# Kernel tuning notes

Measured on AMD Instinct MI355X. Metric: run time of the kernel, lower is better.

## Reference

```python
import jax, jax.numpy as jnp
import numpy as np

HID = 2048      # hidden_size
H = 16          # num query heads
KV = 4          # num kv heads
HD = HID // H   # head_dim = 128
THETA = 1000000.0
T = 2048        # tokens (single causal sequence)


def _rope(x, positions):
    # neox-style rotate-half RoPE over full head_dim. x: [T, h, HD]
    half = HD // 2
    inv_freq = THETA ** (-jnp.arange(half, dtype=jnp.float32) * 2.0 / HD)  # [half]
    freqs = positions.astype(jnp.float32)[:, None] * inv_freq              # [T, half]
    cos = jnp.cos(freqs)[:, None, :]
    sin = jnp.sin(freqs)[:, None, :]
    x1, x2 = x[..., :half], x[..., half:]
    return jnp.concatenate([x1 * cos - x2 * sin, x2 * cos + x1 * sin], axis=-1)


def setup_inputs() -> dict:
    key = jax.random.key(0)
    k1, k2, k3 = jax.random.split(key, 3)
    hidden_states = jax.random.normal(k1, (T, HID), jnp.float32) * 0.02
    w_qkv = jax.random.normal(k2, (HID, (H + 2 * KV) * HD), jnp.float32) * 0.02
    w_o = jax.random.normal(k3, (H * HD, HID), jnp.float32) * 0.02
    positions = jnp.arange(T, dtype=jnp.int32)
    return {"hidden_states": hidden_states, "w_qkv": w_qkv, "w_o": w_o,
            "positions": positions}


def reference(hidden_states, w_qkv, w_o, positions):
    q_size, kv_size = H * HD, KV * HD
    qkv = hidden_states @ w_qkv                                  # [T, q+2kv]
    q = qkv[:, :q_size].reshape(T, H, HD)
    k = qkv[:, q_size:q_size + kv_size].reshape(T, KV, HD)
    v = qkv[:, q_size + kv_size:].reshape(T, KV, HD)
    q = _rope(q, positions)
    k = _rope(k, positions)
    # GQA: expand kv heads to query heads
    group = H // KV
    k_e = jnp.repeat(k, group, axis=1)                           # [T, H, HD]
    v_e = jnp.repeat(v, group, axis=1)
    scale = HD ** -0.5
    scores = jnp.einsum('thd,shd->hts', q, k_e) * scale          # [H, T, T]
    causal = positions[:, None] >= positions[None, :]            # [T, T]
    scores = jnp.where(causal[None, :, :], scores, -1e30)
    attn = jax.nn.softmax(scores, axis=-1)
    o = jnp.einsum('hts,shd->thd', attn, v_e).reshape(T, H * HD)
    return o @ w_o
```

## Files before the change

kernel.cpp:

```cpp
#include <hip/hip_runtime.h>
#include <hip/hip_bf16.h>

#define T_LEN 2048
#define HID 2048
#define NH 16
#define NKV 4
#define HD 128
#define QKV_COLS 3072

typedef __attribute__((ext_vector_type(8))) short bf16x8;
typedef __attribute__((ext_vector_type(4))) float f32x4;

static __device__ __forceinline__ ushort f2bf(float f) {
  __hip_bfloat16 h = __float2bfloat16(f);
  return *reinterpret_cast<ushort*>(&h);
}
static __device__ __forceinline__ float bf2f(ushort u) {
  union { unsigned int i; float f; } v;
  v.i = ((unsigned int)u) << 16;
  return v.f;
}

static __device__ __forceinline__ void async_copy16(const ushort* g, ushort* l) {
  __builtin_amdgcn_global_load_lds(
      (const __attribute__((address_space(1))) unsigned int*)g,
      (__attribute__((address_space(3))) unsigned int*)l, 16, 0, 0);
}

__global__ __launch_bounds__(256) void prep(
    const float* __restrict__ hidden, ushort* __restrict__ hb,
    const float* __restrict__ w_qkv, ushort* __restrict__ wqkvT,
    const int* __restrict__ positions, float2* __restrict__ tbl) {
  __shared__ float t[64][65];
  const int b = blockIdx.x;
  const int tid = threadIdx.x;
  if (b < 4096) {
    int idx = (b * 256 + tid) * 4;
    float4 v = *(const float4*)(hidden + idx);
    ushort4 o;
    o.x = f2bf(v.x); o.y = f2bf(v.y); o.z = f2bf(v.z); o.w = f2bf(v.w);
    *(ushort4*)(hb + idx) = o;
  } else if (b < 5632) {
    const int tb = b - 4096;
    const int bk = (tb & 31) * 64, bn = (tb >> 5) * 64;
    const int c = tid & 63;
#pragma unroll
    for (int i = 0; i < 16; ++i) {
      int r = (tid >> 6) + i * 4;
      t[r][c] = w_qkv[(size_t)(bk + r) * QKV_COLS + bn + c];
    }
    __syncthreads();
#pragma unroll
    for (int i = 0; i < 16; ++i) {
      int r = (tid >> 6) + i * 4;
      wqkvT[(size_t)(bn + r) * HID + bk + c] = f2bf(t[c][r]);
    }
  } else {
    const int rb = b - 5632;
    const int tt = rb * 4 + (tid >> 6), j = tid & 63;
    double inv_freq = pow(1000000.0, -(double)(2 * j) / 128.0);
    double ang = (double)positions[tt] * inv_freq;
    double s, c2;
    sincos(ang, &s, &c2);
    tbl[(size_t)tt * 64 + j] = make_float2((float)c2, (float)s);
  }
}

__global__ __launch_bounds__(256) void transpose_cast(
    const float* __restrict__ W, ushort* __restrict__ WT, int K, int N) {
  __shared__ float t[64][65];
  const int bk = blockIdx.x * 64, bn = blockIdx.y * 64;
  const int tid = threadIdx.x;
  const int c = tid & 63;
#pragma unroll
  for (int i = 0; i < 16; ++i) {
    int r = (tid >> 6) + i * 4;
    t[r][c] = W[(size_t)(bk + r) * N + bn + c];
  }
  __syncthreads();
#pragma unroll
  for (int i = 0; i < 16; ++i) {
    int r = (tid >> 6) + i * 4;
    WT[(size_t)(bn + r) * K + bk + c] = f2bf(t[c][r]);
  }
}

template <bool OUT_BF16>
__global__ __launch_bounds__(256, 3) void gemm_bt(
    const ushort* __restrict__ A, const ushort* __restrict__ BT,
    void* __restrict__ C, int M, int N, int K) {
  __shared__ __align__(16) ushort lds[2][1536 * 8];
  const int tid = threadIdx.x;
  const int bm = blockIdx.y * 64, bn = blockIdx.x * 128;
  const int wave = tid >> 6, lane = tid & 63;
  const int lr = lane & 15, lq = lane >> 4;
  const int wm = (wave & 1) * 32, wn = (wave >> 1) * 64;

  f32x4 acc[2][4];
#pragma unroll
  for (int i = 0; i < 2; ++i)
#pragma unroll
    for (int j = 0; j < 4; ++j) {
      acc[i][j][0] = 0.f; acc[i][j][1] = 0.f;
      acc[i][j][2] = 0.f; acc[i][j][3] = 0.f;
    }

  auto stage = [&](int k0, int buf) {
#pragma unroll
    for (int it = 0; it < 2; ++it) {
      int c = it * 256 + tid;
      int row = c >> 3, sl = c & 7, kc = sl ^ (row & 7);
      async_copy16(A + (size_t)(bm + row) * K + k0 + kc * 8, &lds[buf][c * 8]);
    }
#pragma unroll
    for (int it = 0; it < 4; ++it) {
      int c = it * 256 + tid;
      int row = c >> 3, sl = c & 7, kc = sl ^ (row & 7);
      async_copy16(BT + (size_t)(bn + row) * K + k0 + kc * 8,
                   &lds[buf][(512 + c) * 8]);
    }
  };

  stage(0, 0);
  __syncthreads();
  int cur = 0;
  for (int k0 = 0; k0 < K; k0 += 64) {
    if (k0 + 64 < K) stage(k0 + 64, cur ^ 1);
#pragma unroll
    for (int ks = 0; ks < 2; ++ks) {
      bf16x8 af[2], bfr[4];
#pragma unroll
      for (int mi = 0; mi < 2; ++mi) {
        int row = wm + mi * 16 + lr, kc = ks * 4 + lq;
        af[mi] = *(const bf16x8*)&lds[cur][(row * 8 + (kc ^ (row & 7))) * 8];
      }
#pragma unroll
      for (int ni = 0; ni < 4; ++ni) {
        int row = wn + ni * 16 + lr, kc = ks * 4 + lq;
        bfr[ni] =
            *(const bf16x8*)&lds[cur][(512 + row * 8 + (kc ^ (row & 7))) * 8];
      }
#pragma unroll
      for (int mi = 0; mi < 2; ++mi)
#pragma unroll
        for (int ni = 0; ni < 4; ++ni)
          acc[mi][ni] = __builtin_amdgcn_mfma_f32_16x16x32_bf16(
              af[mi], bfr[ni], acc[mi][ni], 0, 0, 0);
    }
    __syncthreads();
    cur ^= 1;
  }

#pragma unroll
  for (int mi = 0; mi < 2; ++mi)
#pragma unroll
    for (int ni = 0; ni < 4; ++ni)
#pragma unroll
      for (int r = 0; r < 4; ++r) {
        size_t row = bm + wm + mi * 16 + lq * 4 + r;
        size_t col = bn + wn + ni * 16 + lr;
        if (OUT_BF16)
          ((ushort*)C)[row * N + col] = f2bf(acc[mi][ni][r]);
        else
          ((float*)C)[row * N + col] = acc[mi][ni][r];
      }
}

__global__ __launch_bounds__(256, 3) void gemm_qkv(
    const ushort* __restrict__ A, const ushort* __restrict__ BT,
    ushort* __restrict__ qkvb, ushort* __restrict__ vt,
    const float2* __restrict__ tbl, int M, int N, int K) {
  __shared__ __align__(16) ushort lds[2][1536 * 8];
  const int tid = threadIdx.x;
  const int bm = blockIdx.y * 64, bn = blockIdx.x * 128;
  const int wave = tid >> 6, lane = tid & 63;
  const int lr = lane & 15, lq = lane >> 4;
  const int wm = (wave & 1) * 32, wn = (wave >> 1) * 64;

  f32x4 acc[2][4];
#pragma unroll
  for (int i = 0; i < 2; ++i)
#pragma unroll
    for (int j = 0; j < 4; ++j) {
      acc[i][j][0] = 0.f; acc[i][j][1] = 0.f;
      acc[i][j][2] = 0.f; acc[i][j][3] = 0.f;
    }

  auto stage = [&](int k0, int buf) {
#pragma unroll
    for (int it = 0; it < 2; ++it) {
      int c = it * 256 + tid;
      int row = c >> 3, sl = c & 7, kc = sl ^ (row & 7);
      async_copy16(A + (size_t)(bm + row) * K + k0 + kc * 8, &lds[buf][c * 8]);
    }
#pragma unroll
    for (int it = 0; it < 4; ++it) {
      int c = it * 256 + tid;
      int row = c >> 3, sl = c & 7, kc = sl ^ (row & 7);
      async_copy16(BT + (size_t)(bn + row) * K + k0 + kc * 8,
                   &lds[buf][(512 + c) * 8]);
    }
  };

  stage(0, 0);
  __syncthreads();
  int cur = 0;
  for (int k0 = 0; k0 < K; k0 += 64) {
    if (k0 + 64 < K) stage(k0 + 64, cur ^ 1);
#pragma unroll
    for (int ks = 0; ks < 2; ++ks) {
      bf16x8 af[2], bfr[4];
#pragma unroll
      for (int mi = 0; mi < 2; ++mi) {
        int row = wm + mi * 16 + lr, kc = ks * 4 + lq;
        af[mi] = *(const bf16x8*)&lds[cur][(row * 8 + (kc ^ (row & 7))) * 8];
      }
#pragma unroll
      for (int ni = 0; ni < 4; ++ni) {
        int row = wn + ni * 16 + lr, kc = ks * 4 + lq;
        bfr[ni] =
            *(const bf16x8*)&lds[cur][(512 + row * 8 + (kc ^ (row & 7))) * 8];
      }
#pragma unroll
      for (int mi = 0; mi < 2; ++mi)
#pragma unroll
        for (int ni = 0; ni < 4; ++ni)
          acc[mi][ni] = __builtin_amdgcn_mfma_f32_16x16x32_bf16(
              af[mi], bfr[ni], acc[mi][ni], 0, 0, 0);
    }
    __syncthreads();
    cur ^= 1;
  }

  const int head = bn >> 7;
  ushort* ep = &lds[0][0];
  if (head < 20) {
#pragma unroll
    for (int mi = 0; mi < 2; ++mi)
#pragma unroll
      for (int ni = 0; ni < 4; ++ni)
#pragma unroll
        for (int r = 0; r < 4; ++r)
          ep[(wm + mi * 16 + lq * 4 + r) * 130 + wn + ni * 16 + lr] =
              f2bf(acc[mi][ni][r]);
    __syncthreads();

    const float qs = (head < NH) ? 0.08838834764831845f : 1.0f;
#pragma unroll
    for (int it = 0; it < 16; ++it) {
      int idx = it * 256 + tid;
      int row = idx >> 6, j = idx & 63;
      float x1 = bf2f(ep[row * 130 + j]);
      float x2 = bf2f(ep[row * 130 + 64 + j]);
      float2 cs = tbl[(size_t)(bm + row) * 64 + j];
      qkvb[(size_t)(bm + row) * QKV_COLS + bn + j] =
          f2bf((x1 * cs.x - x2 * cs.y) * qs);
      qkvb[(size_t)(bm + row) * QKV_COLS + bn + 64 + j] =
          f2bf((x2 * cs.x + x1 * cs.y) * qs);
    }
  } else {
#pragma unroll
    for (int mi = 0; mi < 2; ++mi)
#pragma unroll
      for (int ni = 0; ni < 4; ++ni)
#pragma unroll
        for (int r = 0; r < 4; ++r)
          ep[(wm + mi * 16 + lq * 4 + r) * 130 + wn + ni * 16 + lr] =
              f2bf(acc[mi][ni][r]);
    __syncthreads();

    const int vd0 = bn - 2560;
#pragma unroll
    for (int it = 0; it < 8; ++it) {
      int idx = it * 256 + tid;
      int vd = idx >> 4, tg = (idx & 15) * 4;
      ushort4 w;
      w.x = ep[(tg + 0) * 130 + vd];
      w.y = ep[(tg + 1) * 130 + vd];
      w.z = ep[(tg + 2) * 130 + vd];
      w.w = ep[(tg + 3) * 130 + vd];
      *(ushort4*)&vt[(size_t)(vd0 + vd) * T_LEN + bm + tg] = w;
    }
  }
}

__global__ __launch_bounds__(256, 3) void attn_mfma(
    const ushort* __restrict__ qkv, const ushort* __restrict__ vt,
    ushort* __restrict__ o, ushort* __restrict__ partials,
    float* __restrict__ ml) {
  int qt, h, k_begin, k_end, slot = -1;
  {
    const int i = blockIdx.x;
    if (i < 512) {
      qt = 31 - (i >> 5);
      const int rem = i & 31;
      h = rem >> 1;
      const int chunk = rem & 1;
      const int n = qt + 1, half = n >> 1;
      k_begin = chunk ? half : 0;
      k_end = chunk ? n : half;
      slot = ((qt - 16) * 16 + h) * 2 + chunk;
    } else {
      const int j = i - 512;
      qt = 15 - (j >> 4);
      h = j & 15;
      k_begin = 0;
      k_end = qt + 1;
    }
  }
  const int kh = h >> 2;
  const int tid = threadIdx.x;
  const int wave = tid >> 6, lane = tid & 63;
  const int lr = lane & 15, lq = lane >> 4;
  const int wq = wave >> 1, ws = wave & 1;

  __shared__ __align__(16) ushort KsL[1024 * 8];
  __shared__ __align__(16) ushort VtsL[1024 * 8];
  __shared__ __align__(16) ushort Ps[8 * 67 * 8];
  __shared__ float l_sh[64][2];

  bf16x8 qf[2][4];
  {
    const ushort* qbase =
        qkv + (size_t)(qt * 64 + wq * 32 + lr) * QKV_COLS + h * HD + lq * 8;
#pragma unroll
    for (int mi = 0; mi < 2; ++mi)
#pragma unroll
      for (int kk = 0; kk < 4; ++kk)
        qf[mi][kk] = *(const bf16x8*)(qbase + (size_t)mi * 16 * QKV_COLS + kk * 32);
  }

  float l_part[2][4];
#pragma unroll
  for (int mi = 0; mi < 2; ++mi)
#pragma unroll
    for (int r = 0; r < 4; ++r) l_part[mi][r] = 0.f;
  f32x4 o_acc[4][2];
#pragma unroll
  for (int qi = 0; qi < 4; ++qi)
#pragma unroll
    for (int di = 0; di < 2; ++di) {
      o_acc[qi][di][0] = 0.f; o_acc[qi][di][1] = 0.f;
      o_acc[qi][di][2] = 0.f; o_acc[qi][di][3] = 0.f;
    }

  for (int kt = k_begin; kt < k_end; ++kt) {
    __syncthreads();

    {
      const ushort* kbase = qkv + 2048 + kh * HD;
#pragma unroll
      for (int it = 0; it < 4; ++it) {
        int c = it * 256 + tid;
        int s = c >> 4, sl = c & 15, dg = sl ^ (s & 15);
        async_copy16(kbase + (size_t)(kt * 64 + s) * QKV_COLS + dg * 8,
                     &KsL[c * 8]);
      }
    }
    {
      const ushort* vbase = vt + (size_t)(kh * HD) * T_LEN + kt * 64;
#pragma unroll
      for (int it = 0; it < 4; ++it) {
        int c = it * 256 + tid;
        int d = c >> 3, sl = c & 7, sc = sl ^ (d & 7);
        async_copy16(vbase + (size_t)d * T_LEN + sc * 8, &VtsL[c * 8]);
      }
    }
    __syncthreads();

    f32x4 s_acc[2][2];
#pragma unroll
    for (int mi = 0; mi < 2; ++mi)
#pragma unroll
      for (int ni = 0; ni < 2; ++ni) {
        s_acc[mi][ni][0] = 0.f; s_acc[mi][ni][1] = 0.f;
        s_acc[mi][ni][2] = 0.f; s_acc[mi][ni][3] = 0.f;
      }
#pragma unroll
    for (int kk = 0; kk < 4; ++kk) {
      bf16x8 kf[2];
#pragma unroll
      for (int ni = 0; ni < 2; ++ni) {
        int s = ws * 32 + ni * 16 + lr;
        kf[ni] = *(const bf16x8*)&KsL[(s * 16 + ((kk * 4 + lq) ^ (s & 15))) * 8];
      }
#pragma unroll
      for (int mi = 0; mi < 2; ++mi)
#pragma unroll
        for (int ni = 0; ni < 2; ++ni)
          s_acc[mi][ni] = __builtin_amdgcn_mfma_f32_16x16x32_bf16(
              qf[mi][kk], kf[ni], s_acc[mi][ni], 0, 0, 0);
    }

    if (kt == qt) {
#pragma unroll
      for (int mi = 0; mi < 2; ++mi)
#pragma unroll
        for (int ni = 0; ni < 2; ++ni)
#pragma unroll
          for (int r = 0; r < 4; ++r)
            if (ws * 32 + ni * 16 + lr > wq * 32 + mi * 16 + lq * 4 + r)
              s_acc[mi][ni][r] = -1e30f;
    }

#pragma unroll
    for (int mi = 0; mi < 2; ++mi)
#pragma unroll
      for (int ni = 0; ni < 2; ++ni)
#pragma unroll
        for (int r = 0; r < 4; ++r) {
          float p = __expf(s_acc[mi][ni][r]);
          l_part[mi][r] += p;
          int s = ws * 32 + ni * 16 + lr;
          int q = wq * 32 + mi * 16 + lq * 4 + r;
          Ps[((s >> 3) * 67 + q) * 8 + (s & 7)] = f2bf(p);
        }
    __syncthreads();

#pragma unroll
    for (int ss = 0; ss < 2; ++ss) {
      bf16x8 vf[2];
#pragma unroll
      for (int di = 0; di < 2; ++di) {
        int d = wave * 32 + di * 16 + lr, sc = ss * 4 + lq;
        vf[di] = *(const bf16x8*)&VtsL[(d * 8 + (sc ^ (d & 7))) * 8];
      }
#pragma unroll
      for (int qi = 0; qi < 4; ++qi) {
        bf16x8 pf = *(const bf16x8*)&Ps[((ss * 4 + lq) * 67 + qi * 16 + lr) * 8];
#pragma unroll
        for (int di = 0; di < 2; ++di)
          o_acc[qi][di] = __builtin_amdgcn_mfma_f32_16x16x32_bf16(
              pf, vf[di], o_acc[qi][di], 0, 0, 0);
      }
    }
  }

#pragma unroll
  for (int mi = 0; mi < 2; ++mi)
#pragma unroll
    for (int r = 0; r < 4; ++r) {
      float v = l_part[mi][r];
#pragma unroll
      for (int off = 1; off < 16; off <<= 1) v += __shfl_xor(v, off, 16);
      l_part[mi][r] = v;
    }
  if (lr == 0) {
#pragma unroll
    for (int mi = 0; mi < 2; ++mi)
#pragma unroll
      for (int r = 0; r < 4; ++r)
        l_sh[wq * 32 + mi * 16 + lq * 4 + r][ws] = l_part[mi][r];
  }
  __syncthreads();

  if (slot < 0) {
    ushort* ob = o + (size_t)(qt * 64) * (NH * HD) + h * HD + wave * 32;
#pragma unroll
    for (int qi = 0; qi < 4; ++qi)
#pragma unroll
      for (int r = 0; r < 4; ++r) {
        int q = qi * 16 + lq * 4 + r;
        float inv = 1.f / (l_sh[q][0] + l_sh[q][1]);
#pragma unroll
        for (int di = 0; di < 2; ++di)
          ob[(size_t)q * (NH * HD) + di * 16 + lr] =
              f2bf(o_acc[qi][di][r] * inv);
      }
  } else {
    ushort* pb = partials + (size_t)slot * 64 * HD + wave * 32;
#pragma unroll
    for (int qi = 0; qi < 4; ++qi)
#pragma unroll
      for (int r = 0; r < 4; ++r) {
        int q = qi * 16 + lq * 4 + r;
#pragma unroll
        for (int di = 0; di < 2; ++di)
          pb[(size_t)q * HD + di * 16 + lr] = f2bf(o_acc[qi][di][r]);
      }
    if (tid < 64) ml[(size_t)slot * 64 + tid] = l_sh[tid][0] + l_sh[tid][1];
  }
}

__global__ __launch_bounds__(256) void attn_reduce(
    const ushort* __restrict__ partials, const float* __restrict__ ml,
    ushort* __restrict__ o) {
  const int bi = blockIdx.x;
  const int qt = 16 + (bi >> 4), h = bi & 15;
  const int s0 = ((qt - 16) * 16 + h) * 2;
  const int tid = threadIdx.x;
  const int row = tid >> 2;
  const int dq = (tid & 3) * 32;

  float l0 = ml[(size_t)s0 * 64 + row];
  float l1 = ml[(size_t)(s0 + 1) * 64 + row];
  float inv = 1.f / (l0 + l1);

  const ushort* p0 = partials + ((size_t)s0 * 64 + row) * HD + dq;
  const ushort* p1 = partials + ((size_t)(s0 + 1) * 64 + row) * HD + dq;
  ushort* ob = o + (size_t)(qt * 64 + row) * (NH * HD) + h * HD + dq;
#pragma unroll
  for (int k = 0; k < 32; ++k)
    ob[k] = f2bf((bf2f(p0[k]) + bf2f(p1[k])) * inv);
}

extern "C" void kernel_launch(void* const* d_in, const int* in_sizes, int n_in,
                              void* d_out, int out_size, void* d_ws,
                              size_t ws_size, hipStream_t stream) {
  const float* hidden = (const float*)d_in[0];
  const float* w_qkv  = (const float*)d_in[1];
  const float* w_o    = (const float*)d_in[2];
  const int* positions = (const int*)d_in[3];
  float* out = (float*)d_out;

  ushort* ws = (ushort*)d_ws;
  ushort* hb    = ws;
  ushort* wqkvT = ws + 4194304;
  ushort* qkvb  = wqkvT + 6291456;
  ushort* vtb   = qkvb + 6291456;
  float*  mlb   = (float*)(vtb + 1048576);
  float2* tbl   = (float2*)(mlb + 32768);
  ushort* ob       = hb;
  ushort* partials = wqkvT;
  ushort* woT      = wqkvT;

  prep<<<6144, 256, 0, stream>>>(hidden, hb, w_qkv, wqkvT, positions, tbl);

  gemm_qkv<<<dim3(QKV_COLS / 128, T_LEN / 64), 256, 0, stream>>>(
      hb, wqkvT, qkvb, vtb, tbl, T_LEN, QKV_COLS, HID);

  attn_mfma<<<768, 256, 0, stream>>>(qkvb, vtb, ob, partials, mlb);
  attn_reduce<<<256, 256, 0, stream>>>(partials, mlb, ob);

  transpose_cast<<<dim3(HID / 64, HID / 64), 256, 0, stream>>>(
      w_o, woT, HID, HID);

  gemm_bt<false><<<dim3(HID / 128, T_LEN / 64), 256, 0, stream>>>(
      ob, woT, out, T_LEN, HID, NH * HD);
}
```

Measured before the change: 203.8 us.

## Load K and V fragments directly from global memory, double-buffer P tile

```diff
diff --git a/kernel.cpp b/kernel.cpp
--- a/kernel.cpp
+++ b/kernel.cpp
@@ -284,7 +284,7 @@
   }
 }
 
-__global__ __launch_bounds__(256, 3) void attn_mfma(
+__global__ __launch_bounds__(256, 4) void attn_mfma(
     const ushort* __restrict__ qkv, const ushort* __restrict__ vt,
     ushort* __restrict__ o, ushort* __restrict__ partials,
     float* __restrict__ ml) {
@@ -314,9 +314,7 @@
   const int lr = lane & 15, lq = lane >> 4;
   const int wq = wave >> 1, ws = wave & 1;
 
-  __shared__ __align__(16) ushort KsL[1024 * 8];
-  __shared__ __align__(16) ushort VtsL[1024 * 8];
-  __shared__ __align__(16) ushort Ps[8 * 67 * 8];
+  __shared__ __align__(16) ushort Ps[2][8 * 67 * 8];
   __shared__ float l_sh[64][2];
 
   bf16x8 qf[2][4];
@@ -344,30 +342,11 @@
       o_acc[qi][di][2] = 0.f; o_acc[qi][di][3] = 0.f;
     }
 
+  const ushort* kbase0 = qkv + 2048 + kh * HD + (size_t)(ws * 32 + lr) * QKV_COLS;
+  const ushort* vbase0 = vt + (size_t)(kh * HD + wave * 32 + lr) * T_LEN;
+
+  int pb = 0;
   for (int kt = k_begin; kt < k_end; ++kt) {
-    __syncthreads();
-
-    {
-      const ushort* kbase = qkv + 2048 + kh * HD;
-#pragma unroll
-      for (int it = 0; it < 4; ++it) {
-        int c = it * 256 + tid;
-        int s = c >> 4, sl = c & 15, dg = sl ^ (s & 15);
-        async_copy16(kbase + (size_t)(kt * 64 + s) * QKV_COLS + dg * 8,
-                     &KsL[c * 8]);
-      }
-    }
-    {
-      const ushort* vbase = vt + (size_t)(kh * HD) * T_LEN + kt * 64;
-#pragma unroll
-      for (int it = 0; it < 4; ++it) {
-        int c = it * 256 + tid;
-        int d = c >> 3, sl = c & 7, sc = sl ^ (d & 7);
-        async_copy16(vbase + (size_t)d * T_LEN + sc * 8, &VtsL[c * 8]);
-      }
-    }
-    __syncthreads();
-
     f32x4 s_acc[2][2];
 #pragma unroll
     for (int mi = 0; mi < 2; ++mi)
@@ -376,20 +355,21 @@
         s_acc[mi][ni][0] = 0.f; s_acc[mi][ni][1] = 0.f;
         s_acc[mi][ni][2] = 0.f; s_acc[mi][ni][3] = 0.f;
       }
-#pragma unroll
-    for (int kk = 0; kk < 4; ++kk) {
-      bf16x8 kf[2];
-#pragma unroll
-      for (int ni = 0; ni < 2; ++ni) {
-        int s = ws * 32 + ni * 16 + lr;
-        kf[ni] = *(const bf16x8*)&KsL[(s * 16 + ((kk * 4 + lq) ^ (s & 15))) * 8];
-      }
-#pragma unroll
-      for (int mi = 0; mi < 2; ++mi)
+    {
+      const ushort* kb = kbase0 + (size_t)(kt * 64) * QKV_COLS + lq * 8;
+#pragma unroll
+      for (int kk = 0; kk < 4; ++kk) {
+        bf16x8 kf[2];
 #pragma unroll
         for (int ni = 0; ni < 2; ++ni)
-          s_acc[mi][ni] = __builtin_amdgcn_mfma_f32_16x16x32_bf16(
-              qf[mi][kk], kf[ni], s_acc[mi][ni], 0, 0, 0);
+          kf[ni] = *(const bf16x8*)(kb + (size_t)(ni * 16) * QKV_COLS + kk * 32);
+#pragma unroll
+        for (int mi = 0; mi < 2; ++mi)
+#pragma unroll
+          for (int ni = 0; ni < 2; ++ni)
+            s_acc[mi][ni] = __builtin_amdgcn_mfma_f32_16x16x32_bf16(
+                qf[mi][kk], kf[ni], s_acc[mi][ni], 0, 0, 0);
+      }
     }
 
     if (kt == qt) {
@@ -413,27 +393,30 @@
           l_part[mi][r] += p;
           int s = ws * 32 + ni * 16 + lr;
           int q = wq * 32 + mi * 16 + lq * 4 + r;
-          Ps[((s >> 3) * 67 + q) * 8 + (s & 7)] = f2bf(p);
+          Ps[pb][((s >> 3) * 67 + q) * 8 + (s & 7)] = f2bf(p);
         }
     __syncthreads();
 
-#pragma unroll
-    for (int ss = 0; ss < 2; ++ss) {
-      bf16x8 vf[2];
-#pragma unroll
-      for (int di = 0; di < 2; ++di) {
-        int d = wave * 32 + di * 16 + lr, sc = ss * 4 + lq;
-        vf[di] = *(const bf16x8*)&VtsL[(d * 8 + (sc ^ (d & 7))) * 8];
-      }
-#pragma unroll
-      for (int qi = 0; qi < 4; ++qi) {
-        bf16x8 pf = *(const bf16x8*)&Ps[((ss * 4 + lq) * 67 + qi * 16 + lr) * 8];
+    {
+      const ushort* vb = vbase0 + kt * 64 + lq * 8;
+#pragma unroll
+      for (int ss = 0; ss < 2; ++ss) {
+        bf16x8 vf[2];
 #pragma unroll
         for (int di = 0; di < 2; ++di)
-          o_acc[qi][di] = __builtin_amdgcn_mfma_f32_16x16x32_bf16(
-              pf, vf[di], o_acc[qi][di], 0, 0, 0);
-      }
-    }
+          vf[di] = *(const bf16x8*)(vb + (size_t)(di * 16) * T_LEN + ss * 32);
+#pragma unroll
+        for (int qi = 0; qi < 4; ++qi) {
+          bf16x8 pf =
+              *(const bf16x8*)&Ps[pb][((ss * 4 + lq) * 67 + qi * 16 + lr) * 8];
+#pragma unroll
+          for (int di = 0; di < 2; ++di)
+            o_acc[qi][di] = __builtin_amdgcn_mfma_f32_16x16x32_bf16(
+                pf, vf[di], o_acc[qi][di], 0, 0, 0);
+        }
+      }
+    }
+    pb ^= 1;
   }
 
 #pragma unroll
@@ -468,7 +451,7 @@
               f2bf(o_acc[qi][di][r] * inv);
       }
   } else {
-    ushort* pb = partials + (size_t)slot * 64 * HD + wave * 32;
+    ushort* pb2 = partials + (size_t)slot * 64 * HD + wave * 32;
 #pragma unroll
     for (int qi = 0; qi < 4; ++qi)
 #pragma unroll
@@ -476,7 +459,7 @@
         int q = qi * 16 + lq * 4 + r;
 #pragma unroll
         for (int di = 0; di < 2; ++di)
-          pb[(size_t)q * HD + di * 16 + lr] = f2bf(o_acc[qi][di][r]);
+          pb2[(size_t)q * HD + di * 16 + lr] = f2bf(o_acc[qi][di][r]);
       }
     if (tid < 64) ml[(size_t)slot * 64 + tid] = l_sh[tid][0] + l_sh[tid][1];
   }
```

New measurement: 235.9 us. +15.8%, slower.

## Enlarge GEMM tiles to 128x128 and drop LDS double buffering

Applied to the files above, without the earlier changes.

```diff
diff --git a/kernel.cpp b/kernel.cpp
--- a/kernel.cpp
+++ b/kernel.cpp
@@ -89,70 +89,63 @@
 __global__ __launch_bounds__(256, 3) void gemm_bt(
     const ushort* __restrict__ A, const ushort* __restrict__ BT,
     void* __restrict__ C, int M, int N, int K) {
-  __shared__ __align__(16) ushort lds[2][1536 * 8];
+  __shared__ __align__(16) ushort lds[2048 * 8];
   const int tid = threadIdx.x;
-  const int bm = blockIdx.y * 64, bn = blockIdx.x * 128;
+  const int bm = blockIdx.y * 128, bn = blockIdx.x * 128;
   const int wave = tid >> 6, lane = tid & 63;
   const int lr = lane & 15, lq = lane >> 4;
-  const int wm = (wave & 1) * 32, wn = (wave >> 1) * 64;
-
-  f32x4 acc[2][4];
-#pragma unroll
-  for (int i = 0; i < 2; ++i)
+  const int wm = (wave & 1) * 64, wn = (wave >> 1) * 64;
+
+  f32x4 acc[4][4];
+#pragma unroll
+  for (int i = 0; i < 4; ++i)
 #pragma unroll
     for (int j = 0; j < 4; ++j) {
       acc[i][j][0] = 0.f; acc[i][j][1] = 0.f;
       acc[i][j][2] = 0.f; acc[i][j][3] = 0.f;
     }
 
-  auto stage = [&](int k0, int buf) {
-#pragma unroll
-    for (int it = 0; it < 2; ++it) {
+  for (int k0 = 0; k0 < K; k0 += 64) {
+#pragma unroll
+    for (int it = 0; it < 4; ++it) {
       int c = it * 256 + tid;
       int row = c >> 3, sl = c & 7, kc = sl ^ (row & 7);
-      async_copy16(A + (size_t)(bm + row) * K + k0 + kc * 8, &lds[buf][c * 8]);
+      async_copy16(A + (size_t)(bm + row) * K + k0 + kc * 8, &lds[c * 8]);
     }
 #pragma unroll
     for (int it = 0; it < 4; ++it) {
       int c = it * 256 + tid;
       int row = c >> 3, sl = c & 7, kc = sl ^ (row & 7);
       async_copy16(BT + (size_t)(bn + row) * K + k0 + kc * 8,
-                   &lds[buf][(512 + c) * 8]);
-    }
-  };
-
-  stage(0, 0);
-  __syncthreads();
-  int cur = 0;
-  for (int k0 = 0; k0 < K; k0 += 64) {
-    if (k0 + 64 < K) stage(k0 + 64, cur ^ 1);
+                   &lds[(1024 + c) * 8]);
+    }
+    __syncthreads();
+
 #pragma unroll
     for (int ks = 0; ks < 2; ++ks) {
-      bf16x8 af[2], bfr[4];
-#pragma unroll
-      for (int mi = 0; mi < 2; ++mi) {
+      bf16x8 af[4], bfr[4];
+#pragma unroll
+      for (int mi = 0; mi < 4; ++mi) {
         int row = wm + mi * 16 + lr, kc = ks * 4 + lq;
-        af[mi] = *(const bf16x8*)&lds[cur][(row * 8 + (kc ^ (row & 7))) * 8];
+        af[mi] = *(const bf16x8*)&lds[(row * 8 + (kc ^ (row & 7))) * 8];
       }
 #pragma unroll
       for (int ni = 0; ni < 4; ++ni) {
         int row = wn + ni * 16 + lr, kc = ks * 4 + lq;
-        bfr[ni] =
-            *(const bf16x8*)&lds[cur][(512 + row * 8 + (kc ^ (row & 7))) * 8];
-      }
-#pragma unroll
-      for (int mi = 0; mi < 2; ++mi)
+        bfr[ni] = *(const bf16x8*)&lds[(1024 + row * 8 + (kc ^ (row & 7))) * 8];
+      }
+#pragma unroll
+      for (int mi = 0; mi < 4; ++mi)
 #pragma unroll
         for (int ni = 0; ni < 4; ++ni)
           acc[mi][ni] = __builtin_amdgcn_mfma_f32_16x16x32_bf16(
               af[mi], bfr[ni], acc[mi][ni], 0, 0, 0);
     }
     __syncthreads();
-    cur ^= 1;
-  }
-
-#pragma unroll
-  for (int mi = 0; mi < 2; ++mi)
+  }
+
+#pragma unroll
+  for (int mi = 0; mi < 4; ++mi)
 #pragma unroll
     for (int ni = 0; ni < 4; ++ni)
 #pragma unroll
@@ -170,84 +163,77 @@
     const ushort* __restrict__ A, const ushort* __restrict__ BT,
     ushort* __restrict__ qkvb, ushort* __restrict__ vt,
     const float2* __restrict__ tbl, int M, int N, int K) {
-  __shared__ __align__(16) ushort lds[2][1536 * 8];
+  __shared__ __align__(16) ushort lds[16640];
   const int tid = threadIdx.x;
-  const int bm = blockIdx.y * 64, bn = blockIdx.x * 128;
+  const int bm = blockIdx.y * 128, bn = blockIdx.x * 128;
   const int wave = tid >> 6, lane = tid & 63;
   const int lr = lane & 15, lq = lane >> 4;
-  const int wm = (wave & 1) * 32, wn = (wave >> 1) * 64;
-
-  f32x4 acc[2][4];
-#pragma unroll
-  for (int i = 0; i < 2; ++i)
+  const int wm = (wave & 1) * 64, wn = (wave >> 1) * 64;
+
+  f32x4 acc[4][4];
+#pragma unroll
+  for (int i = 0; i < 4; ++i)
 #pragma unroll
     for (int j = 0; j < 4; ++j) {
       acc[i][j][0] = 0.f; acc[i][j][1] = 0.f;
       acc[i][j][2] = 0.f; acc[i][j][3] = 0.f;
     }
 
-  auto stage = [&](int k0, int buf) {
-#pragma unroll
-    for (int it = 0; it < 2; ++it) {
+  for (int k0 = 0; k0 < K; k0 += 64) {
+#pragma unroll
+    for (int it = 0; it < 4; ++it) {
       int c = it * 256 + tid;
       int row = c >> 3, sl = c & 7, kc = sl ^ (row & 7);
-      async_copy16(A + (size_t)(bm + row) * K + k0 + kc * 8, &lds[buf][c * 8]);
+      async_copy16(A + (size_t)(bm + row) * K + k0 + kc * 8, &lds[c * 8]);
     }
 #pragma unroll
     for (int it = 0; it < 4; ++it) {
       int c = it * 256 + tid;
       int row = c >> 3, sl = c & 7, kc = sl ^ (row & 7);
       async_copy16(BT + (size_t)(bn + row) * K + k0 + kc * 8,
-                   &lds[buf][(512 + c) * 8]);
-    }
-  };
-
-  stage(0, 0);
-  __syncthreads();
-  int cur = 0;
-  for (int k0 = 0; k0 < K; k0 += 64) {
-    if (k0 + 64 < K) stage(k0 + 64, cur ^ 1);
+                   &lds[(1024 + c) * 8]);
+    }
+    __syncthreads();
+
 #pragma unroll
     for (int ks = 0; ks < 2; ++ks) {
-      bf16x8 af[2], bfr[4];
-#pragma unroll
-      for (int mi = 0; mi < 2; ++mi) {
+      bf16x8 af[4], bfr[4];
+#pragma unroll
+      for (int mi = 0; mi < 4; ++mi) {
         int row = wm + mi * 16 + lr, kc = ks * 4 + lq;
-        af[mi] = *(const bf16x8*)&lds[cur][(row * 8 + (kc ^ (row & 7))) * 8];
+        af[mi] = *(const bf16x8*)&lds[(row * 8 + (kc ^ (row & 7))) * 8];
       }
 #pragma unroll
       for (int ni = 0; ni < 4; ++ni) {
         int row = wn + ni * 16 + lr, kc = ks * 4 + lq;
-        bfr[ni] =
-            *(const bf16x8*)&lds[cur][(512 + row * 8 + (kc ^ (row & 7))) * 8];
-      }
-#pragma unroll
-      for (int mi = 0; mi < 2; ++mi)
+        bfr[ni] = *(const bf16x8*)&lds[(1024 + row * 8 + (kc ^ (row & 7))) * 8];
+      }
+#pragma unroll
+      for (int mi = 0; mi < 4; ++mi)
 #pragma unroll
         for (int ni = 0; ni < 4; ++ni)
           acc[mi][ni] = __builtin_amdgcn_mfma_f32_16x16x32_bf16(
               af[mi], bfr[ni], acc[mi][ni], 0, 0, 0);
     }
     __syncthreads();
-    cur ^= 1;
   }
 
   const int head = bn >> 7;
-  ushort* ep = &lds[0][0];
+  ushort* ep = lds;
+#pragma unroll
+  for (int mi = 0; mi < 4; ++mi)
+#pragma unroll
+    for (int ni = 0; ni < 4; ++ni)
+#pragma unroll
+      for (int r = 0; r < 4; ++r)
+        ep[(wm + mi * 16 + lq * 4 + r) * 130 + wn + ni * 16 + lr] =
+            f2bf(acc[mi][ni][r]);
+  __syncthreads();
+
   if (head < 20) {
-#pragma unroll
-    for (int mi = 0; mi < 2; ++mi)
-#pragma unroll
-      for (int ni = 0; ni < 4; ++ni)
-#pragma unroll
-        for (int r = 0; r < 4; ++r)
-          ep[(wm + mi * 16 + lq * 4 + r) * 130 + wn + ni * 16 + lr] =
-              f2bf(acc[mi][ni][r]);
-    __syncthreads();
-
     const float qs = (head < NH) ? 0.08838834764831845f : 1.0f;
 #pragma unroll
-    for (int it = 0; it < 16; ++it) {
+    for (int it = 0; it < 32; ++it) {
       int idx = it * 256 + tid;
       int row = idx >> 6, j = idx & 63;
       float x1 = bf2f(ep[row * 130 + j]);
@@ -259,21 +245,11 @@
           f2bf((x2 * cs.x + x1 * cs.y) * qs);
     }
   } else {
-#pragma unroll
-    for (int mi = 0; mi < 2; ++mi)
-#pragma unroll
-      for (int ni = 0; ni < 4; ++ni)
-#pragma unroll
-        for (int r = 0; r < 4; ++r)
-          ep[(wm + mi * 16 + lq * 4 + r) * 130 + wn + ni * 16 + lr] =
-              f2bf(acc[mi][ni][r]);
-    __syncthreads();
-
     const int vd0 = bn - 2560;
 #pragma unroll
-    for (int it = 0; it < 8; ++it) {
+    for (int it = 0; it < 16; ++it) {
       int idx = it * 256 + tid;
-      int vd = idx >> 4, tg = (idx & 15) * 4;
+      int vd = idx >> 5, tg = (idx & 31) * 4;
       ushort4 w;
       w.x = ep[(tg + 0) * 130 + vd];
       w.y = ep[(tg + 1) * 130 + vd];
@@ -526,7 +502,7 @@
 
   prep<<<6144, 256, 0, stream>>>(hidden, hb, w_qkv, wqkvT, positions, tbl);
 
-  gemm_qkv<<<dim3(QKV_COLS / 128, T_LEN / 64), 256, 0, stream>>>(
+  gemm_qkv<<<dim3(QKV_COLS / 128, T_LEN / 128), 256, 0, stream>>>(
       hb, wqkvT, qkvb, vtb, tbl, T_LEN, QKV_COLS, HID);
 
   attn_mfma<<<768, 256, 0, stream>>>(qkvb, vtb, ob, partials, mlb);
@@ -535,6 +511,6 @@
   transpose_cast<<<dim3(HID / 64, HID / 64), 256, 0, stream>>>(
       w_o, woT, HID, HID);
 
-  gemm_bt<false><<<dim3(HID / 128, T_LEN / 64), 256, 0, stream>>>(
+  gemm_bt<false><<<dim3(HID / 128, T_LEN / 128), 256, 0, stream>>>(
       ob, woT, out, T_LEN, HID, NH * HD);
 }
```

Result: slower. 222.0 us (+8.9%).
